# Kernel optimization log

Hardware: AMD Instinct MI355X
Metric: run time of the kernel (lower is better)

## Reference

```python
import jax, jax.numpy as jnp
import numpy as np

B = 2048       # batch
POOL = 512     # e_prompt_pool_size
TOPK = 4       # top_k
EPL = 8        # e_prompt_length
GPL = 8        # g_prompt_length
EMB = 768      # emb_d
KEYD = 768     # key_dim


def setup_inputs() -> dict:
    key = jax.random.key(0)
    k1, k2, k3, k4, k5 = jax.random.split(key, 5)
    return {
        "x_querry": jax.random.normal(k1, (B, KEYD), dtype=jnp.float32),
        "x_block": jax.random.normal(k2, (B, EMB), dtype=jnp.float32),
        "e_k": jax.random.uniform(k3, (POOL, KEYD), dtype=jnp.float32),
        "e_p": jax.random.uniform(k4, (POOL, EPL, EMB), dtype=jnp.float32),
        "g_p": jax.random.uniform(k5, (GPL, EMB), dtype=jnp.float32),
        "l": 0,
    }


def _l2norm(x, eps=1e-12):
    # matches torch F.normalize(dim=-1): x / max(||x||, eps)
    n = jnp.sqrt(jnp.sum(x * x, axis=-1, keepdims=True))
    return x / jnp.maximum(n, eps)


def reference(x_querry, x_block, e_k, e_p, g_p, l):
    # ---- E-prompt routing (l in e_layers) ----
    n_K = _l2norm(e_k)                              # [P, C]
    q = jax.lax.stop_gradient(_l2norm(x_querry))    # [B, C], detached in torch
    cos_sim = jnp.einsum('bj,kj->bk', q, n_K)       # [B, P]
    distance = 1.0 - cos_sim
    # use_contrastiv=False -> mass = 1.0
    scaled_distance = distance * 1.0
    # torch.topk(largest=False) == top_k of negated values
    _, k_idx = jax.lax.top_k(-scaled_distance, TOPK)   # [B, K]
    P_ = e_p[k_idx]                                  # [B, K, EPL, EMB] gather
    # non-contrastive loss: (1 - cos_sim[:, k_idx]).mean() -> [B, B, K] mean
    loss = jnp.mean(1.0 - cos_sim[:, k_idx])
    i = EPL // 2
    Ek = P_[:, :, :i, :].reshape(B, -1, EMB)         # [B, K*i, EMB]
    Ev = P_[:, :, i:, :].reshape(B, -1, EMB)
    # count scatter (train_count update)
    counts = jnp.bincount(k_idx.reshape(-1), length=POOL)

    # ---- G-prompt (l in g_layers) ----
    j = GPL // 2
    Gk = jnp.broadcast_to(g_p[:j], (B, j, EMB))
    Gv = jnp.broadcast_to(g_p[j:], (B, GPL - j, EMB))

    Pk = jnp.concatenate([Ek, Gk], axis=1)           # [B, K*i + j, EMB]
    Pv = jnp.concatenate([Ev, Gv], axis=1)
    return Pk, Pv, loss, counts, x_block
```

## Files before the change

kernel.cpp:

```cpp
#include <hip/hip_runtime.h>
#include <math.h>

static constexpr int NB    = 2048;
static constexpr int NPOOL = 512;
static constexpr int NTOPK = 4;
static constexpr int NEPL  = 8;
static constexpr int NEMB  = 768;
static constexpr int NSLOT = 20;

typedef unsigned short u16;
typedef __attribute__((ext_vector_type(8))) short bf16x8;
typedef __attribute__((ext_vector_type(4))) float f32x4;

__global__ __launch_bounds__(256) void norms_kernel(
    const float* __restrict__ xq, const float* __restrict__ ek,
    double* __restrict__ qn, double* __restrict__ kn,
    float* __restrict__ rqn, float* __restrict__ rkn,
    u16* __restrict__ xqh, u16* __restrict__ xql,
    u16* __restrict__ ekh, u16* __restrict__ ekl) {
  int row = blockIdx.x;
  const float* src;
  double* dst;
  float* rdst;
  u16* hh;
  u16* ll;
  if (row < NB) {
    src = xq + (size_t)row * NEMB; dst = qn + row; rdst = rqn + row;
    hh = xqh ? xqh + (size_t)row * NEMB : nullptr;
    ll = xql ? xql + (size_t)row * NEMB : nullptr;
  } else {
    int r = row - NB;
    src = ek + (size_t)r * NEMB; dst = kn + r; rdst = rkn + r;
    hh = ekh ? ekh + (size_t)r * NEMB : nullptr;
    ll = ekl ? ekl + (size_t)r * NEMB : nullptr;
  }
  double s = 0.0;
  for (int i = threadIdx.x; i < NEMB; i += 256) {
    float a = src[i];
    s += (double)a * (double)a;
    if (hh) {
      unsigned u = __float_as_uint(a);
      unsigned r = u + 0x7fff + ((u >> 16) & 1);
      u16 h = (u16)(r >> 16);
      float hf = __uint_as_float((unsigned)h << 16);
      float res = a - hf;
      unsigned ul = __float_as_uint(res);
      unsigned rl = ul + 0x7fff + ((ul >> 16) & 1);
      hh[i] = h;
      ll[i] = (u16)(rl >> 16);
    }
  }
  for (int off = 32; off > 0; off >>= 1) s += __shfl_down(s, off, 64);
  __shared__ double red[4];
  if ((threadIdx.x & 63) == 0) red[threadIdx.x >> 6] = s;
  __syncthreads();
  if (threadIdx.x == 0) {
    double n = sqrt(red[0] + red[1] + red[2] + red[3]);
    *dst = n;
    *rdst = (float)(1.0 / fmax(n, 1e-12));
  }
}

__global__ __launch_bounds__(512) void cos_mfma_kernel(
    const u16* __restrict__ xqh, const u16* __restrict__ xql,
    const u16* __restrict__ ekh, const u16* __restrict__ ekl,
    const float* __restrict__ rqn, const float* __restrict__ rkn,
    float* __restrict__ cosm) {
  const int t = threadIdx.x;
  const int lane = t & 63, w = t >> 6;
  const int mw = (w & 3) * 16;
  const int nh = (w >> 2) * 32;
  const int bp = blockIdx.x * 64, bb = blockIdx.y * 64;
  const int lr = lane & 15, kg = (lane >> 4) * 8;
  const size_t arow  = (size_t)(bb + mw + lr) * NEMB + kg;
  const size_t brow0 = (size_t)(bp + nh + lr) * NEMB + kg;
  const size_t brow1 = (size_t)(bp + nh + 16 + lr) * NEMB + kg;
  const u16* pah  = xqh + arow;
  const u16* pal  = xql + arow;
  const u16* pb0h = ekh + brow0;
  const u16* pb0l = ekl + brow0;
  const u16* pb1h = ekh + brow1;
  const u16* pb1l = ekl + brow1;
  f32x4 acc0 = {0.f, 0.f, 0.f, 0.f};
  f32x4 acc1 = {0.f, 0.f, 0.f, 0.f};

  bf16x8 ah  = *(const bf16x8*)(pah);
  bf16x8 al  = *(const bf16x8*)(pal);
  bf16x8 b0h = *(const bf16x8*)(pb0h);
  bf16x8 b0l = *(const bf16x8*)(pb0l);
  bf16x8 b1h = *(const bf16x8*)(pb1h);
  bf16x8 b1l = *(const bf16x8*)(pb1l);
#pragma unroll
  for (int ks = 1; ks <= NEMB / 32; ks++) {
    bf16x8 nah, nal, nb0h, nb0l, nb1h, nb1l;
    if (ks < NEMB / 32) {
      const int o = ks * 32;
      nah  = *(const bf16x8*)(pah + o);
      nal  = *(const bf16x8*)(pal + o);
      nb0h = *(const bf16x8*)(pb0h + o);
      nb0l = *(const bf16x8*)(pb0l + o);
      nb1h = *(const bf16x8*)(pb1h + o);
      nb1l = *(const bf16x8*)(pb1l + o);
    }
    acc0 = __builtin_amdgcn_mfma_f32_16x16x32_bf16(ah, b0h, acc0, 0, 0, 0);
    acc1 = __builtin_amdgcn_mfma_f32_16x16x32_bf16(ah, b1h, acc1, 0, 0, 0);
    acc0 = __builtin_amdgcn_mfma_f32_16x16x32_bf16(ah, b0l, acc0, 0, 0, 0);
    acc1 = __builtin_amdgcn_mfma_f32_16x16x32_bf16(ah, b1l, acc1, 0, 0, 0);
    acc0 = __builtin_amdgcn_mfma_f32_16x16x32_bf16(al, b0h, acc0, 0, 0, 0);
    acc1 = __builtin_amdgcn_mfma_f32_16x16x32_bf16(al, b1h, acc1, 0, 0, 0);
    if (ks < NEMB / 32) {
      ah = nah; al = nal; b0h = nb0h; b0l = nb0l; b1h = nb1h; b1l = nb1l;
    }
  }
  const float rk0 = rkn[bp + nh + lr];
  const float rk1 = rkn[bp + nh + 16 + lr];
  const int r0 = bb + mw + (lane >> 4) * 4;
#pragma unroll
  for (int j = 0; j < 4; j++) {
    const float rq = rqn[r0 + j];
    cosm[(size_t)(r0 + j) * NPOOL + bp + nh + lr]      = acc0[j] * rq * rk0;
    cosm[(size_t)(r0 + j) * NPOOL + bp + nh + 16 + lr] = acc1[j] * rq * rk1;
  }
}

__global__ __launch_bounds__(256) void cos_kernel(
    const float* __restrict__ xq, const float* __restrict__ ek,
    const float* __restrict__ rqn, const float* __restrict__ rkn,
    float* __restrict__ cosm) {
  __shared__ float As[32][68];
  __shared__ float Bs[32][68];
  const int t = threadIdx.x;
  const int tx = t & 15;
  const int ty = t >> 4;
  const int bp = blockIdx.x * 64;
  const int bb = blockIdx.y * 64;
  float acc[4][4] = {};
  for (int k0 = 0; k0 < NEMB; k0 += 32) {
#pragma unroll
    for (int uu = 0; uu < 2; uu++) {
      int u = t + uu * 256;
      int m = u >> 3;
      int k4 = (u & 7) * 4;
      float4 a = *(const float4*)(xq + (size_t)(bb + m) * NEMB + k0 + k4);
      float4 b = *(const float4*)(ek + (size_t)(bp + m) * NEMB + k0 + k4);
      As[k4 + 0][m] = a.x; As[k4 + 1][m] = a.y; As[k4 + 2][m] = a.z; As[k4 + 3][m] = a.w;
      Bs[k4 + 0][m] = b.x; Bs[k4 + 1][m] = b.y; Bs[k4 + 2][m] = b.z; Bs[k4 + 3][m] = b.w;
    }
    __syncthreads();
#pragma unroll
    for (int kk = 0; kk < 32; kk++) {
      float4 av = *(const float4*)&As[kk][ty * 4];
      float4 bv = *(const float4*)&Bs[kk][tx * 4];
      acc[0][0] = fmaf(av.x, bv.x, acc[0][0]); acc[0][1] = fmaf(av.x, bv.y, acc[0][1]);
      acc[0][2] = fmaf(av.x, bv.z, acc[0][2]); acc[0][3] = fmaf(av.x, bv.w, acc[0][3]);
      acc[1][0] = fmaf(av.y, bv.x, acc[1][0]); acc[1][1] = fmaf(av.y, bv.y, acc[1][1]);
      acc[1][2] = fmaf(av.y, bv.z, acc[1][2]); acc[1][3] = fmaf(av.y, bv.w, acc[1][3]);
      acc[2][0] = fmaf(av.z, bv.x, acc[2][0]); acc[2][1] = fmaf(av.z, bv.y, acc[2][1]);
      acc[2][2] = fmaf(av.z, bv.z, acc[2][2]); acc[2][3] = fmaf(av.z, bv.w, acc[2][3]);
      acc[3][0] = fmaf(av.w, bv.x, acc[3][0]); acc[3][1] = fmaf(av.w, bv.y, acc[3][1]);
      acc[3][2] = fmaf(av.w, bv.z, acc[3][2]); acc[3][3] = fmaf(av.w, bv.w, acc[3][3]);
    }
    __syncthreads();
  }
  float4 rk = *(const float4*)&rkn[bp + tx * 4];
#pragma unroll
  for (int i = 0; i < 4; i++) {
    float rq = rqn[bb + ty * 4 + i];
    float4 cv;
    cv.x = acc[i][0] * rq * rk.x;
    cv.y = acc[i][1] * rq * rk.y;
    cv.z = acc[i][2] * rq * rk.z;
    cv.w = acc[i][3] * rq * rk.w;
    *(float4*)(cosm + (size_t)(bb + ty * 4 + i) * NPOOL + bp + tx * 4) = cv;
  }
}

__device__ __forceinline__ bool btf(float av, int ai, float bv, int bi) {
  return (av > bv) || (av == bv && ai < bi);
}
__device__ __forceinline__ bool btd(double av, int ai, double bv, int bi) {
  return (av > bv) || (av == bv && ai < bi);
}
#define CE(a, b)                                                        \
  do {                                                                  \
    if (!btf(v[a], vi[a], v[b], vi[b])) {                               \
      float tv = v[a]; v[a] = v[b]; v[b] = tv;                          \
      int ti = vi[a]; vi[a] = vi[b]; vi[b] = ti;                        \
    }                                                                   \
  } while (0)

__global__ __launch_bounds__(256) void topk_kernel(
    const float* __restrict__ cosm, const float* __restrict__ xq,
    const float* __restrict__ ek, const double* __restrict__ qn,
    const double* __restrict__ kn, int* __restrict__ kidx,
    int* __restrict__ counts) {
  int wave = threadIdx.x >> 6, lane = threadIdx.x & 63;
  int row = blockIdx.x * 4 + wave;
  const float* crow = cosm + (size_t)row * NPOOL;
  float v[8]; int vi[8];
#pragma unroll
  for (int j = 0; j < 8; j++) {
    int p = j * 64 + lane;
    v[j] = crow[p];
    vi[j] = p;
  }
  CE(0,1); CE(2,3); CE(4,5); CE(6,7);
  CE(0,2); CE(1,3); CE(4,6); CE(5,7);
  CE(1,2); CE(5,6);
  CE(0,4); CE(1,5); CE(2,6); CE(3,7);
  CE(2,4); CE(3,5);
  CE(1,2); CE(3,4); CE(5,6);
#pragma unroll
  for (int off = 1; off < 64; off <<= 1) {
    float ov[8]; int oi[8];
#pragma unroll
    for (int m = 0; m < 8; m++) {
      ov[m] = __shfl_xor(v[m], off, 64);
      oi[m] = __shfl_xor(vi[m], off, 64);
    }
#pragma unroll
    for (int m = 0; m < 8; m++) {
      if (!btf(v[m], vi[m], ov[7 - m], oi[7 - m])) { v[m] = ov[7 - m]; vi[m] = oi[7 - m]; }
    }
    CE(0,4); CE(1,5); CE(2,6); CE(3,7);
    CE(0,2); CE(1,3); CE(4,6); CE(5,7);
    CE(0,1); CE(2,3); CE(4,5); CE(6,7);
  }
  const float* xrow = xq + (size_t)row * NEMB;
  double xr[12];
#pragma unroll
  for (int e = 0; e < 12; e++) xr[e] = (double)xrow[lane * 12 + e];
  double qmax = fmax(qn[row], 1e-12);
  double cand[8];
#pragma unroll
  for (int c = 0; c < 8; c++) {
    int pi = vi[c];
    const float* kb = ek + (size_t)pi * NEMB + lane * 12;
    double s = 0.0;
#pragma unroll
    for (int e = 0; e < 12; e++) s = fma(xr[e], (double)kb[e], s);
#pragma unroll
    for (int off = 1; off < 64; off <<= 1) s += __shfl_xor(s, off, 64);
    cand[c] = s / (qmax * fmax(kn[pi], 1e-12));
  }
  bool used[8] = {false, false, false, false, false, false, false, false};
#pragma unroll
  for (int m = 0; m < NTOPK; m++) {
    int best = -1;
#pragma unroll
    for (int c = 0; c < 8; c++) {
      if (!used[c] && (best < 0 || btd(cand[c], vi[c], cand[best], vi[best]))) best = c;
    }
    used[best] = true;
    if (lane == 0) {
      kidx[row * 4 + m] = vi[best];
      atomicAdd(&counts[vi[best]], 1);
    }
  }
}
#undef CE

__global__ __launch_bounds__(256) void colsum_kernel(
    const float* __restrict__ cosm, double* __restrict__ S) {
  int p = blockIdx.x * 256 + threadIdx.x;
  int r0 = blockIdx.y * 128;
  double s = 0.0;
  for (int r = r0; r < r0 + 128; r++) s += (double)cosm[(size_t)r * NPOOL + p];
  atomicAdd(&S[p], s);
}

__global__ __launch_bounds__(256) void loss_counts_kernel(
    const double* __restrict__ S, const int* __restrict__ counts,
    float* __restrict__ out_loss, float* __restrict__ out_counts) {
  double s = 0.0;
  for (int p = threadIdx.x; p < NPOOL; p += 256) {
    int c = counts[p];
    out_counts[p] = (float)c;
    s += (double)c * S[p];
  }
  for (int off = 32; off > 0; off >>= 1) s += __shfl_down(s, off, 64);
  __shared__ double red[4];
  if ((threadIdx.x & 63) == 0) red[threadIdx.x >> 6] = s;
  __syncthreads();
  if (threadIdx.x == 0) {
    double total = red[0] + red[1] + red[2] + red[3];
    *out_loss = (float)(1.0 - total / (double)((long long)NB * NB * NTOPK));
  }
}

__global__ __launch_bounds__(256) void gather_kernel(
    const float* __restrict__ e_p, const float* __restrict__ g_p,
    const int* __restrict__ kidx, const float* __restrict__ x_block,
    float* __restrict__ Pk, float* __restrict__ Pv,
    float* __restrict__ out_xb) {
  int b = blockIdx.x;
  __shared__ int idx[4];
  if (threadIdx.x < 4) idx[threadIdx.x] = kidx[b * 4 + threadIdx.x];
  __syncthreads();
  float4* dk = (float4*)(Pk + (size_t)b * NSLOT * NEMB);
  float4* dv = (float4*)(Pv + (size_t)b * NSLOT * NEMB);
  const int R = NEMB / 4;
  for (int u = threadIdx.x; u < NSLOT * R; u += 256) {
    int s = u / R;
    int r = u - s * R;
    const float4* sk;
    const float4* sv;
    if (s < 16) {
      int pi = idx[s >> 2];
      int t = s & 3;
      const float* basek = e_p + ((size_t)pi * NEPL + t) * NEMB;
      sk = (const float4*)basek;
      sv = (const float4*)(basek + 4 * NEMB);
    } else {
      sk = (const float4*)(g_p + (size_t)(s - 16) * NEMB);
      sv = (const float4*)(g_p + (size_t)(s - 16 + 4) * NEMB);
    }
    dk[u] = sk[r];
    dv[u] = sv[r];
  }
  const float* xsrc = x_block + (size_t)b * NEMB;
  float* xdst = out_xb + (size_t)b * NEMB;
  if (threadIdx.x < 3) xdst[threadIdx.x] = xsrc[threadIdx.x];
  if (threadIdx.x == 3) xdst[NEMB - 1] = xsrc[NEMB - 1];
  for (int k = threadIdx.x; k < 191; k += 256) {
    int i = 3 + 4 * k;
    float4 vv = make_float4(xsrc[i], xsrc[i + 1], xsrc[i + 2], xsrc[i + 3]);
    *(float4*)(xdst + i) = vv;
  }
}

extern "C" void kernel_launch(void* const* d_in, const int* in_sizes, int n_in,
                              void* d_out, int out_size, void* d_ws, size_t ws_size,
                              hipStream_t stream) {
  const float* x_querry = (const float*)d_in[0];
  const float* x_block  = (const float*)d_in[1];
  const float* e_k      = (const float*)d_in[2];
  const float* e_p      = (const float*)d_in[3];
  const float* g_p      = (const float*)d_in[4];

  double* qn     = (double*)d_ws;
  double* kn     = qn + NB;
  double* S      = kn + NPOOL;
  float*  rqn    = (float*)(S + NPOOL);
  float*  rkn    = rqn + NB;
  float*  cosm   = rkn + NPOOL;
  int*    kidx   = (int*)(cosm + (size_t)NB * NPOOL);
  int*    counts = kidx + NB * NTOPK;
  u16*    xqh    = (u16*)(counts + NPOOL);
  u16*    xql    = xqh + (size_t)NB * NEMB;
  u16*    ekh    = xql + (size_t)NB * NEMB;
  u16*    ekl    = ekh + (size_t)NPOOL * NEMB;
  const size_t ws_need =
      (size_t)((char*)(ekl + (size_t)NPOOL * NEMB) - (char*)d_ws);
  const bool use_mfma = ws_size >= ws_need;

  float* out        = (float*)d_out;
  float* Pk         = out;
  float* Pv         = Pk + (size_t)NB * NSLOT * NEMB;
  float* out_loss   = Pv + (size_t)NB * NSLOT * NEMB;
  float* out_counts = out_loss + 1;
  float* out_xb     = out_counts + NPOOL;

  hipMemsetAsync(S, 0, NPOOL * sizeof(double), stream);
  hipMemsetAsync(counts, 0, NPOOL * sizeof(int), stream);

  norms_kernel<<<NB + NPOOL, 256, 0, stream>>>(
      x_querry, e_k, qn, kn, rqn, rkn,
      use_mfma ? xqh : nullptr, use_mfma ? xql : nullptr,
      use_mfma ? ekh : nullptr, use_mfma ? ekl : nullptr);
  if (use_mfma) {
    cos_mfma_kernel<<<dim3(NPOOL / 64, NB / 64), 512, 0, stream>>>(
        xqh, xql, ekh, ekl, rqn, rkn, cosm);
  } else {
    cos_kernel<<<dim3(NPOOL / 64, NB / 64), 256, 0, stream>>>(
        x_querry, e_k, rqn, rkn, cosm);
  }
  topk_kernel<<<NB / 4, 256, 0, stream>>>(cosm, x_querry, e_k, qn, kn, kidx, counts);
  colsum_kernel<<<dim3(NPOOL / 256, NB / 128), 256, 0, stream>>>(cosm, S);
  loss_counts_kernel<<<1, 256, 0, stream>>>(S, counts, out_loss, out_counts);
  gather_kernel<<<NB, 256, 0, stream>>>(e_p, g_p, kidx, x_block, Pk, Pv, out_xb);
}
```

Baseline: 378.7 us.

## Fuse memsets, column sum and loss into neighboring kernels; use nontemporal stores

Zeroing of S and counts moves into an extra block of the norms kernel, replacing two memsets. The column sum of the cosine matrix is computed inside the top-k kernel via shared memory and double atomics, and the loss/counts reduction becomes an extra block of the gather kernel. Gather output stores become nontemporal. This removes launches and a second read of the cosine matrix, but greatly increases atomic traffic on S.

```diff
diff --git a/kernel.cpp b/kernel.cpp
--- a/kernel.cpp
+++ b/kernel.cpp
@@ -17,8 +17,13 @@
     double* __restrict__ qn, double* __restrict__ kn,
     float* __restrict__ rqn, float* __restrict__ rkn,
     u16* __restrict__ xqh, u16* __restrict__ xql,
-    u16* __restrict__ ekh, u16* __restrict__ ekl) {
+    u16* __restrict__ ekh, u16* __restrict__ ekl,
+    double* __restrict__ S, int* __restrict__ counts) {
   int row = blockIdx.x;
+  if (row == NB + NPOOL) {
+    for (int i = threadIdx.x; i < NPOOL; i += 256) { S[i] = 0.0; counts[i] = 0; }
+    return;
+  }
   const float* src;
   double* dst;
   float* rdst;
@@ -189,11 +194,12 @@
     }                                                                   \
   } while (0)
 
-__global__ __launch_bounds__(256) void topk_kernel(
+__global__ __launch_bounds__(256) void topk_colsum_kernel(
     const float* __restrict__ cosm, const float* __restrict__ xq,
     const float* __restrict__ ek, const double* __restrict__ qn,
     const double* __restrict__ kn, int* __restrict__ kidx,
-    int* __restrict__ counts) {
+    int* __restrict__ counts, double* __restrict__ S) {
+  __shared__ double colv[4][NPOOL];
   int wave = threadIdx.x >> 6, lane = threadIdx.x & 63;
   int row = blockIdx.x * 4 + wave;
   const float* crow = cosm + (size_t)row * NPOOL;
@@ -203,6 +209,16 @@
     int p = j * 64 + lane;
     v[j] = crow[p];
     vi[j] = p;
+    colv[wave][p] = (double)v[j];
+  }
+  __syncthreads();
+  {
+    int c = threadIdx.x;
+    double s0 = colv[0][c] + colv[1][c] + colv[2][c] + colv[3][c];
+    int c2 = c + 256;
+    double s1 = colv[0][c2] + colv[1][c2] + colv[2][c2] + colv[3][c2];
+    atomicAdd(&S[c], s0);
+    atomicAdd(&S[c2], s1);
   }
   CE(0,1); CE(2,3); CE(4,5); CE(6,7);
   CE(0,2); CE(1,3); CE(4,6); CE(5,7);
@@ -260,63 +276,58 @@
 }
 #undef CE
 
-__global__ __launch_bounds__(256) void colsum_kernel(
-    const float* __restrict__ cosm, double* __restrict__ S) {
-  int p = blockIdx.x * 256 + threadIdx.x;
-  int r0 = blockIdx.y * 128;
-  double s = 0.0;
-  for (int r = r0; r < r0 + 128; r++) s += (double)cosm[(size_t)r * NPOOL + p];
-  atomicAdd(&S[p], s);
-}
-
-__global__ __launch_bounds__(256) void loss_counts_kernel(
-    const double* __restrict__ S, const int* __restrict__ counts,
-    float* __restrict__ out_loss, float* __restrict__ out_counts) {
-  double s = 0.0;
-  for (int p = threadIdx.x; p < NPOOL; p += 256) {
-    int c = counts[p];
-    out_counts[p] = (float)c;
-    s += (double)c * S[p];
-  }
-  for (int off = 32; off > 0; off >>= 1) s += __shfl_down(s, off, 64);
-  __shared__ double red[4];
-  if ((threadIdx.x & 63) == 0) red[threadIdx.x >> 6] = s;
-  __syncthreads();
-  if (threadIdx.x == 0) {
-    double total = red[0] + red[1] + red[2] + red[3];
-    *out_loss = (float)(1.0 - total / (double)((long long)NB * NB * NTOPK));
-  }
-}
-
-__global__ __launch_bounds__(256) void gather_kernel(
+__device__ __forceinline__ void nt_store4(float* p, f32x4 v) {
+  __builtin_nontemporal_store(v, (f32x4*)p);
+}
+
+__global__ __launch_bounds__(256) void gather_loss_kernel(
     const float* __restrict__ e_p, const float* __restrict__ g_p,
     const int* __restrict__ kidx, const float* __restrict__ x_block,
+    const double* __restrict__ S, const int* __restrict__ counts,
     float* __restrict__ Pk, float* __restrict__ Pv,
-    float* __restrict__ out_xb) {
+    float* __restrict__ out_xb, float* __restrict__ out_loss,
+    float* __restrict__ out_counts) {
   int b = blockIdx.x;
+  if (b == NB) {
+    double s = 0.0;
+    for (int p = threadIdx.x; p < NPOOL; p += 256) {
+      int c = counts[p];
+      out_counts[p] = (float)c;
+      s += (double)c * S[p];
+    }
+    for (int off = 32; off > 0; off >>= 1) s += __shfl_down(s, off, 64);
+    __shared__ double red[4];
+    if ((threadIdx.x & 63) == 0) red[threadIdx.x >> 6] = s;
+    __syncthreads();
+    if (threadIdx.x == 0) {
+      double total = red[0] + red[1] + red[2] + red[3];
+      *out_loss = (float)(1.0 - total / (double)((long long)NB * NB * NTOPK));
+    }
+    return;
+  }
   __shared__ int idx[4];
   if (threadIdx.x < 4) idx[threadIdx.x] = kidx[b * 4 + threadIdx.x];
   __syncthreads();
-  float4* dk = (float4*)(Pk + (size_t)b * NSLOT * NEMB);
-  float4* dv = (float4*)(Pv + (size_t)b * NSLOT * NEMB);
+  float* dk = Pk + (size_t)b * NSLOT * NEMB;
+  float* dv = Pv + (size_t)b * NSLOT * NEMB;
   const int R = NEMB / 4;
   for (int u = threadIdx.x; u < NSLOT * R; u += 256) {
     int s = u / R;
     int r = u - s * R;
-    const float4* sk;
-    const float4* sv;
+    const f32x4* sk;
+    const f32x4* sv;
     if (s < 16) {
       int pi = idx[s >> 2];
       int t = s & 3;
       const float* basek = e_p + ((size_t)pi * NEPL + t) * NEMB;
-      sk = (const float4*)basek;
-      sv = (const float4*)(basek + 4 * NEMB);
+      sk = (const f32x4*)basek;
+      sv = (const f32x4*)(basek + 4 * NEMB);
     } else {
-      sk = (const float4*)(g_p + (size_t)(s - 16) * NEMB);
-      sv = (const float4*)(g_p + (size_t)(s - 16 + 4) * NEMB);
-    }
-    dk[u] = sk[r];
-    dv[u] = sv[r];
+      sk = (const f32x4*)(g_p + (size_t)(s - 16) * NEMB);
+      sv = (const f32x4*)(g_p + (size_t)(s - 16 + 4) * NEMB);
+    }
+    nt_store4(dk + u * 4, sk[r]);
+    nt_store4(dv + u * 4, sv[r]);
   }
   const float* xsrc = x_block + (size_t)b * NEMB;
   float* xdst = out_xb + (size_t)b * NEMB;
@@ -324,8 +335,8 @@
   if (threadIdx.x == 3) xdst[NEMB - 1] = xsrc[NEMB - 1];
   for (int k = threadIdx.x; k < 191; k += 256) {
     int i = 3 + 4 * k;
-    float4 vv = make_float4(xsrc[i], xsrc[i + 1], xsrc[i + 2], xsrc[i + 3]);
-    *(float4*)(xdst + i) = vv;
+    f32x4 vv = {xsrc[i], xsrc[i + 1], xsrc[i + 2], xsrc[i + 3]};
+    nt_store4(xdst + i, vv);
   }
 }
 
@@ -361,13 +372,11 @@
   float* out_counts = out_loss + 1;
   float* out_xb     = out_counts + NPOOL;
 
-  hipMemsetAsync(S, 0, NPOOL * sizeof(double), stream);
-  hipMemsetAsync(counts, 0, NPOOL * sizeof(int), stream);
-
-  norms_kernel<<<NB + NPOOL, 256, 0, stream>>>(
+  norms_kernel<<<NB + NPOOL + 1, 256, 0, stream>>>(
       x_querry, e_k, qn, kn, rqn, rkn,
       use_mfma ? xqh : nullptr, use_mfma ? xql : nullptr,
-      use_mfma ? ekh : nullptr, use_mfma ? ekl : nullptr);
+      use_mfma ? ekh : nullptr, use_mfma ? ekl : nullptr,
+      S, counts);
   if (use_mfma) {
     cos_mfma_kernel<<<dim3(NPOOL / 64, NB / 64), 512, 0, stream>>>(
         xqh, xql, ekh, ekl, rqn, rkn, cosm);
@@ -375,8 +384,8 @@
     cos_kernel<<<dim3(NPOOL / 64, NB / 64), 256, 0, stream>>>(
         x_querry, e_k, rqn, rkn, cosm);
   }
-  topk_kernel<<<NB / 4, 256, 0, stream>>>(cosm, x_querry, e_k, qn, kn, kidx, counts);
-  colsum_kernel<<<dim3(NPOOL / 256, NB / 128), 256, 0, stream>>>(cosm, S);
-  loss_counts_kernel<<<1, 256, 0, stream>>>(S, counts, out_loss, out_counts);
-  gather_kernel<<<NB, 256, 0, stream>>>(e_p, g_p, kidx, x_block, Pk, Pv, out_xb);
-}
+  topk_colsum_kernel<<<NB / 4, 256, 0, stream>>>(
+      cosm, x_querry, e_k, qn, kn, kidx, counts, S);
+  gather_loss_kernel<<<NB + 1, 256, 0, stream>>>(
+      e_p, g_p, kidx, x_block, S, counts, Pk, Pv, out_xb, out_loss, out_counts);
+}
```

New measurement: 368.5 us. 2.7% less time.
